# Kernel optimization log

Measured on AMD Instinct MI355X. Metric: run time of the kernel, lower is better.

Reference implementation:

```python
import jax, jax.numpy as jnp
import numpy as np

NUM_HEADS = 16
DIM_EMBED = 1024
DIM_K = DIM_EMBED // NUM_HEADS


def setup_inputs() -> dict:
    key = jax.random.key(0)
    ks = jax.random.split(key, 11)
    B, S, D = 2, 2048, DIM_EMBED
    scale = 1.0 / np.sqrt(D)
    inp = {
        "query": jax.random.normal(ks[0], (B, S, D), dtype=jnp.float32),
        "key": jax.random.normal(ks[1], (B, S, D), dtype=jnp.float32),
        "value": jax.random.normal(ks[2], (B, S, D), dtype=jnp.float32),
        # torch nn.Linear weights: [out_features, in_features], y = x @ W.T + b
        "Wq": jax.random.normal(ks[3], (D, D), dtype=jnp.float32) * scale,
        "bq": jnp.zeros((D,), dtype=jnp.float32),
        "Wk": jax.random.normal(ks[4], (D, D), dtype=jnp.float32) * scale,
        "bk": jnp.zeros((D,), dtype=jnp.float32),
        "Wv": jax.random.normal(ks[5], (D, D), dtype=jnp.float32) * scale,
        "bv": jnp.zeros((D,), dtype=jnp.float32),
        "Wo": jax.random.normal(ks[6], (D, D), dtype=jnp.float32) * scale,
        "bo": jnp.zeros((D,), dtype=jnp.float32),
    }
    return inp


def _split_heads(x):
    B, S, D = x.shape
    return x.reshape(B, S, NUM_HEADS, DIM_K).transpose(0, 2, 1, 3)  # [B,H,S,dk]


def reference(query, key, value, Wq, bq, Wk, bk, Wv, bv, Wo, bo):
    q = _split_heads(query @ Wq.T + bq)   # [B,H,S,dk]
    k = _split_heads(key @ Wk.T + bk)
    v = _split_heads(value @ Wv.T + bv)
    # reactivity = q @ k^T, scaled AFTER matmul as in the original
    reactivity = jnp.einsum("bhsd,bhtd->bhst", q, k)
    attention_score = jax.nn.softmax(reactivity / np.sqrt(DIM_K), axis=-1)
    blended = jnp.einsum("bhst,bhtd->bhsd", attention_score, v)  # [B,H,S,dk]
    B, H, S, dk = blended.shape
    blended = blended.transpose(0, 2, 1, 3).reshape(B, S, H * dk)
    out = blended @ Wo.T + bo
    return out, attention_score
```

## Files before the change

### kernel.cpp

```cpp
#include <hip/hip_runtime.h>
#include <stdint.h>

#define BATCH 2
#define SEQ   2048
#define DEMB  1024
#define NHEAD 16
#define DK    64
#define NTOK  (BATCH * SEQ)
#define OUT_ELEMS ((size_t)NTOK * DEMB)

typedef __bf16 bf16x8 __attribute__((ext_vector_type(8)));
typedef float  f32x4  __attribute__((ext_vector_type(4)));
union FragU { uint4 u; bf16x8 b; };

__device__ __forceinline__ unsigned short f2bf(float f) {
  union { float f; unsigned u; } v; v.f = f;
  unsigned r = v.u + 0x7fffu + ((v.u >> 16) & 1u);
  return (unsigned short)(r >> 16);
}

__device__ __forceinline__ void gll16(const void* g, void* l) {
  __builtin_amdgcn_global_load_lds(
      (const __attribute__((address_space(1))) void*)g,
      (__attribute__((address_space(3))) void*)l, 16, 0, 0);
}

__global__ __launch_bounds__(256) void k_cvt(
    const float* __restrict__ q, const float* __restrict__ k, const float* __restrict__ v,
    const float* __restrict__ wq, const float* __restrict__ wk,
    const float* __restrict__ wv, const float* __restrict__ wo,
    unsigned short* __restrict__ dq, unsigned short* __restrict__ dk,
    unsigned short* __restrict__ dv, unsigned short* __restrict__ dwq,
    unsigned short* __restrict__ dwk, unsigned short* __restrict__ dwv,
    unsigned short* __restrict__ dwo)
{
  const int t = blockIdx.y;
  const float* s; unsigned short* d; int n4;
  switch (t) {
    case 0: s = q;  d = dq;  n4 = NTOK * DEMB / 4; break;
    case 1: s = k;  d = dk;  n4 = NTOK * DEMB / 4; break;
    case 2: s = v;  d = dv;  n4 = NTOK * DEMB / 4; break;
    case 3: s = wq; d = dwq; n4 = DEMB * DEMB / 4; break;
    case 4: s = wk; d = dwk; n4 = DEMB * DEMB / 4; break;
    case 5: s = wv; d = dwv; n4 = DEMB * DEMB / 4; break;
    default: s = wo; d = dwo; n4 = DEMB * DEMB / 4; break;
  }
  for (int i = blockIdx.x * 256 + threadIdx.x; i < n4; i += gridDim.x * 256) {
    float4 f = ((const float4*)s)[i];
    ushort4 o; o.x = f2bf(f.x); o.y = f2bf(f.y); o.z = f2bf(f.z); o.w = f2bf(f.w);
    ((ushort4*)d)[i] = o;
  }
}

__global__ __launch_bounds__(256) void k_proj(
    const unsigned short* __restrict__ Xqb, const unsigned short* __restrict__ Xkb,
    const unsigned short* __restrict__ Xvb,
    const unsigned short* __restrict__ Wqb, const unsigned short* __restrict__ Wkb,
    const unsigned short* __restrict__ Wvb,
    const float* __restrict__ bq, const float* __restrict__ bk, const float* __restrict__ bv,
    unsigned short* __restrict__ qh, unsigned short* __restrict__ kh,
    unsigned short* __restrict__ vh)
{
  const int p = blockIdx.z;
  const unsigned short* __restrict__ X = (p == 0) ? Xqb : (p == 1) ? Xkb : Xvb;
  const unsigned short* __restrict__ W = (p == 0) ? Wqb : (p == 1) ? Wkb : Wvb;
  const float* __restrict__ bias       = (p == 0) ? bq  : (p == 1) ? bk  : bv;
  unsigned short* __restrict__ dst     = (p == 0) ? qh  : (p == 1) ? kh  : vh;

  __shared__ unsigned short As[128][64];
  __shared__ unsigned short Bs[128][64];

  const int tid  = threadIdx.x;
  const int lane = tid & 63;
  const int w    = tid >> 6;
  const int wm   = (w & 1) * 64;
  const int wn   = (w >> 1) * 64;
  const int l15  = lane & 15;
  const int quad = lane >> 4;

  const int o0  = blockIdx.x * 128;
  const int t0b = blockIdx.y * 128;

  f32x4 acc[4][4];
#pragma unroll
  for (int mi = 0; mi < 4; ++mi)
#pragma unroll
    for (int ni = 0; ni < 4; ++ni) acc[mi][ni] = {0.f, 0.f, 0.f, 0.f};

  for (int kk = 0; kk < DEMB; kk += 64) {
#pragma unroll
    for (int r = 0; r < 4; ++r) {
      int idx = tid + r * 256;
      int row = idx >> 3, c = (idx & 7) * 8;
      gll16(&W[(size_t)(o0 + row) * DEMB + kk + c], (unsigned short*)As + idx * 8);
      gll16(&X[(size_t)(t0b + row) * DEMB + kk + c], (unsigned short*)Bs + idx * 8);
    }
    __syncthreads();
#pragma unroll
    for (int k0 = 0; k0 < 64; k0 += 32) {
      FragU af[4], bfr[4];
#pragma unroll
      for (int mi = 0; mi < 4; ++mi)
        af[mi].u = *(const uint4*)&As[wm + mi * 16 + l15][k0 + quad * 8];
#pragma unroll
      for (int ni = 0; ni < 4; ++ni)
        bfr[ni].u = *(const uint4*)&Bs[wn + ni * 16 + l15][k0 + quad * 8];
#pragma unroll
      for (int mi = 0; mi < 4; ++mi)
#pragma unroll
        for (int ni = 0; ni < 4; ++ni)
          acc[mi][ni] = __builtin_amdgcn_mfma_f32_16x16x32_bf16(af[mi].b, bfr[ni].b, acc[mi][ni], 0, 0, 0);
    }
    __syncthreads();
  }

#pragma unroll
  for (int mi = 0; mi < 4; ++mi) {
    const int ob = o0 + wm + mi * 16 + quad * 4;
    const float4 bi = *(const float4*)&bias[ob];
    const int h_ = ob >> 6, db = ob & 63;
#pragma unroll
    for (int ni = 0; ni < 4; ++ni) {
      int token = t0b + wn + ni * 16 + l15;
      int b_ = token >> 11, s_ = token & 2047;
      ushort4 ov;
      ov.x = f2bf(acc[mi][ni][0] + bi.x);
      ov.y = f2bf(acc[mi][ni][1] + bi.y);
      ov.z = f2bf(acc[mi][ni][2] + bi.z);
      ov.w = f2bf(acc[mi][ni][3] + bi.w);
      *(ushort4*)&dst[(((size_t)b_ * NHEAD + h_) * SEQ + s_) * DK + db] = ov;
    }
  }
}

__global__ __launch_bounds__(256) void k_vt(const unsigned short* __restrict__ vh,
                                            unsigned short* __restrict__ vt)
{
  const int bh = blockIdx.y, s0 = blockIdx.x * 64;
  const size_t hoff = (size_t)bh * SEQ * DK;
  __shared__ unsigned short Ls[64][72];
  const int tid = threadIdx.x;
#pragma unroll
  for (int r = 0; r < 2; ++r) {
    int idx = tid + r * 256, row = idx >> 3, c = (idx & 7) * 8;
    uint4 v = *(const uint4*)&vh[hoff + (size_t)(s0 + row) * DK + c];
    *(uint4*)&Ls[row][c] = v;
  }
  __syncthreads();
#pragma unroll
  for (int r = 0; r < 2; ++r) {
    int idx = tid + r * 256, d = idx >> 3, c = (idx & 7) * 8;
    unsigned short tmp[8];
#pragma unroll
    for (int j = 0; j < 8; ++j) tmp[j] = Ls[c + j][d];
    *(uint4*)&vt[hoff + (size_t)d * SEQ + s0 + c] = *(const uint4*)tmp;
  }
}

__global__ __launch_bounds__(256) void k_attn(
    const unsigned short* __restrict__ qh, const unsigned short* __restrict__ kh,
    const unsigned short* __restrict__ vt, unsigned short* __restrict__ blended,
    float* __restrict__ Pout)
{
  const int bh = blockIdx.y;
  const int s0 = blockIdx.x * 64;
  const size_t hoff = (size_t)bh * SEQ * DK;

  __shared__ unsigned short Qs[64][64];
  __shared__ unsigned short Ks[64][64];
  __shared__ unsigned short Vs[64][64];
  __shared__ unsigned short Ps[64][72];
  __shared__ float rowpart[4][64];
  __shared__ float recipS[64];

  const int tid  = threadIdx.x;
  const int lane = tid & 63;
  const int w    = tid >> 6;
  const int l15  = lane & 15;
  const int quad = lane >> 4;

  gll16(&qh[hoff + (size_t)s0 * DK + (size_t)tid * 8], (unsigned short*)Qs + tid * 8);
  gll16(&qh[hoff + (size_t)s0 * DK + (size_t)(tid + 256) * 8], (unsigned short*)Qs + (tid + 256) * 8);
  __syncthreads();

  FragU qf[4][2];
#pragma unroll
  for (int mi = 0; mi < 4; ++mi)
#pragma unroll
    for (int k0 = 0; k0 < 2; ++k0)
      qf[mi][k0].u = *(const uint4*)&Qs[mi * 16 + l15][k0 * 32 + quad * 8];

  float rs[4] = {0.f, 0.f, 0.f, 0.f};
  for (int t0 = 0; t0 < SEQ; t0 += 64) {
    __syncthreads();
    gll16(&kh[hoff + (size_t)t0 * DK + (size_t)tid * 8], (unsigned short*)Ks + tid * 8);
    gll16(&kh[hoff + (size_t)t0 * DK + (size_t)(tid + 256) * 8], (unsigned short*)Ks + (tid + 256) * 8);
    __syncthreads();
    FragU kf[2];
    kf[0].u = *(const uint4*)&Ks[w * 16 + l15][quad * 8];
    kf[1].u = *(const uint4*)&Ks[w * 16 + l15][32 + quad * 8];
#pragma unroll
    for (int mi = 0; mi < 4; ++mi) {
      f32x4 a = {0.f, 0.f, 0.f, 0.f};
      a = __builtin_amdgcn_mfma_f32_16x16x32_bf16(kf[0].b, qf[mi][0].b, a, 0, 0, 0);
      a = __builtin_amdgcn_mfma_f32_16x16x32_bf16(kf[1].b, qf[mi][1].b, a, 0, 0, 0);
#pragma unroll
      for (int i = 0; i < 4; ++i) rs[mi] += __expf(a[i] * 0.125f);
    }
  }
#pragma unroll
  for (int mi = 0; mi < 4; ++mi) {
    float v = rs[mi];
    v += __shfl_xor(v, 16); v += __shfl_xor(v, 32);
    rs[mi] = v;
  }
  if (lane < 16) {
#pragma unroll
    for (int mi = 0; mi < 4; ++mi) rowpart[w][mi * 16 + lane] = rs[mi];
  }
  __syncthreads();
  if (tid < 64)
    recipS[tid] = 1.0f / (rowpart[0][tid] + rowpart[1][tid] + rowpart[2][tid] + rowpart[3][tid]);
  __syncthreads();
  float rcp[4];
#pragma unroll
  for (int mi = 0; mi < 4; ++mi) rcp[mi] = recipS[mi * 16 + l15];

  f32x4 accpv[4];
#pragma unroll
  for (int mi = 0; mi < 4; ++mi) accpv[mi] = {0.f, 0.f, 0.f, 0.f};

  for (int t0 = 0; t0 < SEQ; t0 += 64) {
    __syncthreads();
    gll16(&kh[hoff + (size_t)t0 * DK + (size_t)tid * 8], (unsigned short*)Ks + tid * 8);
    gll16(&kh[hoff + (size_t)t0 * DK + (size_t)(tid + 256) * 8], (unsigned short*)Ks + (tid + 256) * 8);
    gll16(&vt[hoff + (size_t)(tid >> 3) * SEQ + t0 + (tid & 7) * 8], (unsigned short*)Vs + tid * 8);
    gll16(&vt[hoff + (size_t)((tid + 256) >> 3) * SEQ + t0 + (tid & 7) * 8], (unsigned short*)Vs + (tid + 256) * 8);
    __syncthreads();
    FragU kf[2];
    kf[0].u = *(const uint4*)&Ks[w * 16 + l15][quad * 8];
    kf[1].u = *(const uint4*)&Ks[w * 16 + l15][32 + quad * 8];
#pragma unroll
    for (int mi = 0; mi < 4; ++mi) {
      f32x4 a = {0.f, 0.f, 0.f, 0.f};
      a = __builtin_amdgcn_mfma_f32_16x16x32_bf16(kf[0].b, qf[mi][0].b, a, 0, 0, 0);
      a = __builtin_amdgcn_mfma_f32_16x16x32_bf16(kf[1].b, qf[mi][1].b, a, 0, 0, 0);
      float e0 = __expf(a[0] * 0.125f) * rcp[mi];
      float e1 = __expf(a[1] * 0.125f) * rcp[mi];
      float e2 = __expf(a[2] * 0.125f) * rcp[mi];
      float e3 = __expf(a[3] * 0.125f) * rcp[mi];
      float4 p4; p4.x = e0; p4.y = e1; p4.z = e2; p4.w = e3;
      *(float4*)&Pout[((size_t)bh * SEQ + s0 + mi * 16 + l15) * SEQ + t0 + w * 16 + quad * 4] = p4;
      ushort4 pb; pb.x = f2bf(e0); pb.y = f2bf(e1); pb.z = f2bf(e2); pb.w = f2bf(e3);
      *(ushort4*)&Ps[mi * 16 + l15][w * 16 + quad * 4] = pb;
    }
    __syncthreads();
    FragU vf[2];
    vf[0].u = *(const uint4*)&Vs[w * 16 + l15][quad * 8];
    vf[1].u = *(const uint4*)&Vs[w * 16 + l15][32 + quad * 8];
#pragma unroll
    for (int mi = 0; mi < 4; ++mi) {
      FragU pf0, pf1;
      pf0.u = *(const uint4*)&Ps[mi * 16 + l15][quad * 8];
      pf1.u = *(const uint4*)&Ps[mi * 16 + l15][32 + quad * 8];
      accpv[mi] = __builtin_amdgcn_mfma_f32_16x16x32_bf16(vf[0].b, pf0.b, accpv[mi], 0, 0, 0);
      accpv[mi] = __builtin_amdgcn_mfma_f32_16x16x32_bf16(vf[1].b, pf1.b, accpv[mi], 0, 0, 0);
    }
  }

  const int b_ = bh >> 4, h_ = bh & 15;
#pragma unroll
  for (int mi = 0; mi < 4; ++mi) {
    ushort4 ob;
    ob.x = f2bf(accpv[mi][0]); ob.y = f2bf(accpv[mi][1]);
    ob.z = f2bf(accpv[mi][2]); ob.w = f2bf(accpv[mi][3]);
    int token = b_ * SEQ + s0 + mi * 16 + l15;
    *(ushort4*)&blended[(size_t)token * DEMB + h_ * DK + w * 16 + quad * 4] = ob;
  }
}

__global__ __launch_bounds__(256) void k_outproj(
    const unsigned short* __restrict__ Wob, const unsigned short* __restrict__ blended,
    const float* __restrict__ bo, float* __restrict__ out)
{
  __shared__ unsigned short As[128][64];
  __shared__ unsigned short Bs[128][64];

  const int tid  = threadIdx.x;
  const int lane = tid & 63;
  const int w    = tid >> 6;
  const int wm   = (w & 1) * 64;
  const int wn   = (w >> 1) * 64;
  const int l15  = lane & 15;
  const int quad = lane >> 4;

  const int o0  = blockIdx.x * 128;
  const int t0b = blockIdx.y * 128;

  f32x4 acc[4][4];
#pragma unroll
  for (int mi = 0; mi < 4; ++mi)
#pragma unroll
    for (int ni = 0; ni < 4; ++ni) acc[mi][ni] = {0.f, 0.f, 0.f, 0.f};

  for (int kk = 0; kk < DEMB; kk += 64) {
#pragma unroll
    for (int r = 0; r < 4; ++r) {
      int idx = tid + r * 256;
      int row = idx >> 3, c = (idx & 7) * 8;
      gll16(&Wob[(size_t)(o0 + row) * DEMB + kk + c], (unsigned short*)As + idx * 8);
      gll16(&blended[(size_t)(t0b + row) * DEMB + kk + c], (unsigned short*)Bs + idx * 8);
    }
    __syncthreads();
#pragma unroll
    for (int k0 = 0; k0 < 64; k0 += 32) {
      FragU af[4], bfr[4];
#pragma unroll
      for (int mi = 0; mi < 4; ++mi)
        af[mi].u = *(const uint4*)&As[wm + mi * 16 + l15][k0 + quad * 8];
#pragma unroll
      for (int ni = 0; ni < 4; ++ni)
        bfr[ni].u = *(const uint4*)&Bs[wn + ni * 16 + l15][k0 + quad * 8];
#pragma unroll
      for (int mi = 0; mi < 4; ++mi)
#pragma unroll
        for (int ni = 0; ni < 4; ++ni)
          acc[mi][ni] = __builtin_amdgcn_mfma_f32_16x16x32_bf16(af[mi].b, bfr[ni].b, acc[mi][ni], 0, 0, 0);
    }
    __syncthreads();
  }

#pragma unroll
  for (int mi = 0; mi < 4; ++mi) {
    const int ob = o0 + wm + mi * 16 + quad * 4;
    const float4 bi = *(const float4*)&bo[ob];
#pragma unroll
    for (int ni = 0; ni < 4; ++ni) {
      int token = t0b + wn + ni * 16 + l15;
      float4 ov;
      ov.x = acc[mi][ni][0] + bi.x;
      ov.y = acc[mi][ni][1] + bi.y;
      ov.z = acc[mi][ni][2] + bi.z;
      ov.w = acc[mi][ni][3] + bi.w;
      *(float4*)&out[(size_t)token * DEMB + ob] = ov;
    }
  }
}

extern "C" void kernel_launch(void* const* d_in, const int* in_sizes, int n_in,
                              void* d_out, int out_size, void* d_ws, size_t ws_size,
                              hipStream_t stream) {
  const float* Xq = (const float*)d_in[0];
  const float* Xk = (const float*)d_in[1];
  const float* Xv = (const float*)d_in[2];
  const float* Wq = (const float*)d_in[3];
  const float* bq = (const float*)d_in[4];
  const float* Wk = (const float*)d_in[5];
  const float* bk = (const float*)d_in[6];
  const float* Wv = (const float*)d_in[7];
  const float* bv = (const float*)d_in[8];
  const float* Wo = (const float*)d_in[9];
  const float* bo = (const float*)d_in[10];

  float* out  = (float*)d_out;
  float* Pout = out + OUT_ELEMS;

  unsigned short* Xqb = (unsigned short*)d_ws;
  unsigned short* Xkb = Xqb + OUT_ELEMS;
  unsigned short* Xvb = Xkb + OUT_ELEMS;
  unsigned short* Wqb = Xvb + OUT_ELEMS;
  unsigned short* Wkb = Wqb + (size_t)DEMB * DEMB;
  unsigned short* Wvb = Wkb + (size_t)DEMB * DEMB;
  unsigned short* Wob = Wvb + (size_t)DEMB * DEMB;
  unsigned short* qh      = Wob + (size_t)DEMB * DEMB;
  unsigned short* kh      = qh + OUT_ELEMS;
  unsigned short* vh      = kh + OUT_ELEMS;
  unsigned short* vt      = vh + OUT_ELEMS;
  unsigned short* blended = vt + OUT_ELEMS;

  k_cvt<<<dim3(1024, 7), 256, 0, stream>>>(Xq, Xk, Xv, Wq, Wk, Wv, Wo,
                                           Xqb, Xkb, Xvb, Wqb, Wkb, Wvb, Wob);
  k_proj<<<dim3(8, 32, 3), 256, 0, stream>>>(Xqb, Xkb, Xvb, Wqb, Wkb, Wvb,
                                             bq, bk, bv, qh, kh, vh);
  k_vt<<<dim3(32, 32), 256, 0, stream>>>(vh, vt);
  k_attn<<<dim3(SEQ / 64, BATCH * NHEAD), 256, 0, stream>>>(qh, kh, vt, blended, Pout);
  k_outproj<<<dim3(8, 32), 256, 0, stream>>>(Wob, blended, bo, out);
}
```

Before: 789.4 us.

## Load K/V fragments directly from global, double-buffer and swizzle P tile

The attention kernel stops staging Q, K and V through shared memory. Each wave instead loads its MFMA fragments straight from global memory, which removes two barriers per iteration in both passes. The P tile becomes double-buffered with an XOR swizzle, so only one barrier per iteration remains and LDS bank conflicts drop. It also adds a launch-bounds occupancy hint and partial unrolling. The cost is uncoalesced or redundant per-wave global loads of K and V, which now depend on L2/L1 hits.

```diff
diff --git a/kernel.cpp b/kernel.cpp
--- a/kernel.cpp
+++ b/kernel.cpp
@@ -157,7 +157,7 @@
   }
 }
 
-__global__ __launch_bounds__(256) void k_attn(
+__global__ __launch_bounds__(256, 4) void k_attn(
     const unsigned short* __restrict__ qh, const unsigned short* __restrict__ kh,
     const unsigned short* __restrict__ vt, unsigned short* __restrict__ blended,
     float* __restrict__ Pout)
@@ -166,10 +166,7 @@
   const int s0 = blockIdx.x * 64;
   const size_t hoff = (size_t)bh * SEQ * DK;
 
-  __shared__ unsigned short Qs[64][64];
-  __shared__ unsigned short Ks[64][64];
-  __shared__ unsigned short Vs[64][64];
-  __shared__ unsigned short Ps[64][72];
+  __shared__ unsigned short Ps[2][64][64];
   __shared__ float rowpart[4][64];
   __shared__ float recipS[64];
 
@@ -179,33 +176,29 @@
   const int l15  = lane & 15;
   const int quad = lane >> 4;
 
-  gll16(&qh[hoff + (size_t)s0 * DK + (size_t)tid * 8], (unsigned short*)Qs + tid * 8);
-  gll16(&qh[hoff + (size_t)s0 * DK + (size_t)(tid + 256) * 8], (unsigned short*)Qs + (tid + 256) * 8);
-  __syncthreads();
-
   FragU qf[4][2];
 #pragma unroll
   for (int mi = 0; mi < 4; ++mi)
 #pragma unroll
     for (int k0 = 0; k0 < 2; ++k0)
-      qf[mi][k0].u = *(const uint4*)&Qs[mi * 16 + l15][k0 * 32 + quad * 8];
+      qf[mi][k0].u = *(const uint4*)&qh[hoff + (size_t)(s0 + mi * 16 + l15) * DK + k0 * 32 + quad * 8];
+
+  const unsigned short* kbase = kh + hoff + (size_t)(w * 16 + l15) * DK + quad * 8;
+  const unsigned short* vbase = vt + hoff + (size_t)(w * 16 + l15) * SEQ + quad * 8;
 
   float rs[4] = {0.f, 0.f, 0.f, 0.f};
+#pragma unroll 2
   for (int t0 = 0; t0 < SEQ; t0 += 64) {
-    __syncthreads();
-    gll16(&kh[hoff + (size_t)t0 * DK + (size_t)tid * 8], (unsigned short*)Ks + tid * 8);
-    gll16(&kh[hoff + (size_t)t0 * DK + (size_t)(tid + 256) * 8], (unsigned short*)Ks + (tid + 256) * 8);
-    __syncthreads();
-    FragU kf[2];
-    kf[0].u = *(const uint4*)&Ks[w * 16 + l15][quad * 8];
-    kf[1].u = *(const uint4*)&Ks[w * 16 + l15][32 + quad * 8];
+    FragU kf0, kf1;
+    kf0.u = *(const uint4*)(kbase + (size_t)t0 * DK);
+    kf1.u = *(const uint4*)(kbase + (size_t)t0 * DK + 32);
 #pragma unroll
     for (int mi = 0; mi < 4; ++mi) {
       f32x4 a = {0.f, 0.f, 0.f, 0.f};
-      a = __builtin_amdgcn_mfma_f32_16x16x32_bf16(kf[0].b, qf[mi][0].b, a, 0, 0, 0);
-      a = __builtin_amdgcn_mfma_f32_16x16x32_bf16(kf[1].b, qf[mi][1].b, a, 0, 0, 0);
-#pragma unroll
-      for (int i = 0; i < 4; ++i) rs[mi] += __expf(a[i] * 0.125f);
+      a = __builtin_amdgcn_mfma_f32_16x16x32_bf16(kf0.b, qf[mi][0].b, a, 0, 0, 0);
+      a = __builtin_amdgcn_mfma_f32_16x16x32_bf16(kf1.b, qf[mi][1].b, a, 0, 0, 0);
+      rs[mi] += __expf(a[0] * 0.125f) + __expf(a[1] * 0.125f)
+              + __expf(a[2] * 0.125f) + __expf(a[3] * 0.125f);
     }
   }
 #pragma unroll
@@ -230,21 +223,18 @@
 #pragma unroll
   for (int mi = 0; mi < 4; ++mi) accpv[mi] = {0.f, 0.f, 0.f, 0.f};
 
-  for (int t0 = 0; t0 < SEQ; t0 += 64) {
-    __syncthreads();
-    gll16(&kh[hoff + (size_t)t0 * DK + (size_t)tid * 8], (unsigned short*)Ks + tid * 8);
-    gll16(&kh[hoff + (size_t)t0 * DK + (size_t)(tid + 256) * 8], (unsigned short*)Ks + (tid + 256) * 8);
-    gll16(&vt[hoff + (size_t)(tid >> 3) * SEQ + t0 + (tid & 7) * 8], (unsigned short*)Vs + tid * 8);
-    gll16(&vt[hoff + (size_t)((tid + 256) >> 3) * SEQ + t0 + (tid & 7) * 8], (unsigned short*)Vs + (tid + 256) * 8);
-    __syncthreads();
-    FragU kf[2];
-    kf[0].u = *(const uint4*)&Ks[w * 16 + l15][quad * 8];
-    kf[1].u = *(const uint4*)&Ks[w * 16 + l15][32 + quad * 8];
+  for (int t0 = 0, buf = 0; t0 < SEQ; t0 += 64, buf ^= 1) {
+    FragU kf0, kf1, vf0, vf1;
+    kf0.u = *(const uint4*)(kbase + (size_t)t0 * DK);
+    kf1.u = *(const uint4*)(kbase + (size_t)t0 * DK + 32);
+    vf0.u = *(const uint4*)(vbase + t0);
+    vf1.u = *(const uint4*)(vbase + t0 + 32);
+    unsigned short* Pb = &Ps[buf][0][0];
 #pragma unroll
     for (int mi = 0; mi < 4; ++mi) {
       f32x4 a = {0.f, 0.f, 0.f, 0.f};
-      a = __builtin_amdgcn_mfma_f32_16x16x32_bf16(kf[0].b, qf[mi][0].b, a, 0, 0, 0);
-      a = __builtin_amdgcn_mfma_f32_16x16x32_bf16(kf[1].b, qf[mi][1].b, a, 0, 0, 0);
+      a = __builtin_amdgcn_mfma_f32_16x16x32_bf16(kf0.b, qf[mi][0].b, a, 0, 0, 0);
+      a = __builtin_amdgcn_mfma_f32_16x16x32_bf16(kf1.b, qf[mi][1].b, a, 0, 0, 0);
       float e0 = __expf(a[0] * 0.125f) * rcp[mi];
       float e1 = __expf(a[1] * 0.125f) * rcp[mi];
       float e2 = __expf(a[2] * 0.125f) * rcp[mi];
@@ -252,19 +242,19 @@
       float4 p4; p4.x = e0; p4.y = e1; p4.z = e2; p4.w = e3;
       *(float4*)&Pout[((size_t)bh * SEQ + s0 + mi * 16 + l15) * SEQ + t0 + w * 16 + quad * 4] = p4;
       ushort4 pb; pb.x = f2bf(e0); pb.y = f2bf(e1); pb.z = f2bf(e2); pb.w = f2bf(e3);
-      *(ushort4*)&Ps[mi * 16 + l15][w * 16 + quad * 4] = pb;
-    }
-    __syncthreads();
-    FragU vf[2];
-    vf[0].u = *(const uint4*)&Vs[w * 16 + l15][quad * 8];
-    vf[1].u = *(const uint4*)&Vs[w * 16 + l15][32 + quad * 8];
+      const int row = mi * 16 + l15;
+      const int u   = w * 4 + quad;
+      *(ushort4*)(Pb + row * 64 + ((((u >> 1) ^ (row & 7)) << 3) | ((u & 1) << 2))) = pb;
+    }
+    __syncthreads();
 #pragma unroll
     for (int mi = 0; mi < 4; ++mi) {
+      const int row = mi * 16 + l15;
       FragU pf0, pf1;
-      pf0.u = *(const uint4*)&Ps[mi * 16 + l15][quad * 8];
-      pf1.u = *(const uint4*)&Ps[mi * 16 + l15][32 + quad * 8];
-      accpv[mi] = __builtin_amdgcn_mfma_f32_16x16x32_bf16(vf[0].b, pf0.b, accpv[mi], 0, 0, 0);
-      accpv[mi] = __builtin_amdgcn_mfma_f32_16x16x32_bf16(vf[1].b, pf1.b, accpv[mi], 0, 0, 0);
+      pf0.u = *(const uint4*)(Pb + row * 64 + ((quad ^ (row & 7)) << 3));
+      pf1.u = *(const uint4*)(Pb + row * 64 + (((4 + quad) ^ (row & 7)) << 3));
+      accpv[mi] = __builtin_amdgcn_mfma_f32_16x16x32_bf16(vf0.b, pf0.b, accpv[mi], 0, 0, 0);
+      accpv[mi] = __builtin_amdgcn_mfma_f32_16x16x32_bf16(vf1.b, pf1.b, accpv[mi], 0, 0, 0);
     }
   }
 
```

New measurement: 833.8 us. 5.6% more time.
